# Optimization experiments

Hardware: AMD Instinct MI355X
Metric: run time of the kernel (lower is better)

Reference implementation:

```python
import jax, jax.numpy as jnp
import numpy as np

D = 1024      # d_model
H = 16        # nhead
DH = D // H   # head_dim = 64
ROT = DH // 2 # rotary_ndims = 32
FFN = 4096    # d_ffn
B, T, M, N = 4, 1024, 128, 64


def _layernorm(x, g, b, eps=1e-5):
    mu = jnp.mean(x, axis=-1, keepdims=True)
    var = jnp.mean(jnp.square(x - mu), axis=-1, keepdims=True)
    return (x - mu) * jax.lax.rsqrt(var + eps) * g + b


def _rotate_half(x):
    x1, x2 = x[..., : x.shape[-1] // 2], x[..., x.shape[-1] // 2:]
    return jnp.concatenate([-x2, x1], axis=-1)


def setup_inputs() -> dict:
    key = jax.random.key(0)
    ks = jax.random.split(key, 16)
    s = 0.02
    inp = {
        'x': jax.random.normal(ks[0], (B, T, D), jnp.float32),
        'memory': jax.random.normal(ks[1], (B, M, D), jnp.float32),
        'nmr': jax.random.normal(ks[2], (B, N, D), jnp.float32),
        'Wq': jax.random.normal(ks[3], (D, D), jnp.float32) * s,
        'bq': jnp.zeros((D,), jnp.float32),
        'Wk': jax.random.normal(ks[4], (D, D), jnp.float32) * s,
        'bk': jnp.zeros((D,), jnp.float32),
        'Wv': jax.random.normal(ks[5], (D, D), jnp.float32) * s,
        'bv': jnp.zeros((D,), jnp.float32),
        'Wo': jax.random.normal(ks[6], (D, D), jnp.float32) * s,
        'bo': jnp.zeros((D,), jnp.float32),
        'W1': jax.random.normal(ks[7], (D, FFN), jnp.float32) * s,
        'b1': jnp.zeros((FFN,), jnp.float32),
        'W2': jax.random.normal(ks[8], (FFN, D), jnp.float32) * s,
        'b2': jnp.zeros((D,), jnp.float32),
        'ln1_g': jnp.ones((D,), jnp.float32),
        'ln1_b': jnp.zeros((D,), jnp.float32),
        'ln2_g': jnp.ones((D,), jnp.float32),
        'ln2_b': jnp.zeros((D,), jnp.float32),
    }
    return inp


def reference(x, memory, nmr, Wq, bq, Wk, bk, Wv, bv, Wo, bo, W1, b1, W2, b2,
              ln1_g, ln1_b, ln2_g, ln2_b):
    b, t, _ = x.shape
    m, n = memory.shape[1], nmr.shape[1]
    pref = m + n
    L = pref + t

    x_full = jnp.concatenate([memory, nmr, x], axis=1)  # (B, L, D)
    xa = _layernorm(x_full, ln1_g, ln1_b)

    def heads(w, bias):
        return (xa @ w + bias).reshape(b, L, H, DH).transpose(0, 2, 1, 3)  # (B,H,L,DH)

    q = heads(Wq, bq)
    k = heads(Wk, bk)
    v = heads(Wv, bv)

    # partial RoPE on first ROT dims of each head
    pos = jnp.arange(L, dtype=jnp.float32)
    inv_freq = 1.0 / (10000.0 ** (jnp.arange(0, ROT, 2, dtype=jnp.float32) / ROT))
    freqs = pos[:, None] * inv_freq[None, :]              # (L, ROT/2)
    emb = jnp.concatenate([freqs, freqs], axis=-1)        # (L, ROT)
    cos, sin = jnp.cos(emb), jnp.sin(emb)
    qr, qp = q[..., :ROT], q[..., ROT:]
    kr, kp = k[..., :ROT], k[..., ROT:]
    qr = qr * cos + _rotate_half(qr) * sin
    kr = kr * cos + _rotate_half(kr) * sin
    q = jnp.concatenate([qr, qp], axis=-1)
    k = jnp.concatenate([kr, kp], axis=-1)

    # block mask: prefix (memory+nmr) fully bidirectional, target causal,
    # target attends to full prefix, prefix does NOT attend to target.
    i = jnp.arange(L)
    allowed = (i[None, :] < pref) | ((i[:, None] >= pref) & (i[None, :] >= pref)
                                     & (i[None, :] <= i[:, None]))  # (L, L)

    scale = 1.0 / jnp.sqrt(jnp.asarray(DH, jnp.float32))
    scores = jnp.einsum('bhqd,bhkd->bhqk', q, k) * scale
    scores = jnp.where(allowed[None, None], scores, jnp.finfo(scores.dtype).min)
    probs = jax.nn.softmax(scores, axis=-1)
    attn = jnp.einsum('bhqk,bhkd->bhqd', probs, v)        # (B,H,L,DH)
    attn = attn.transpose(0, 2, 1, 3).reshape(b, L, D)

    x_full = attn @ Wo + bo + x_full

    xf = _layernorm(x_full, ln2_g, ln2_b)
    xf = jnp.square(jax.nn.relu(xf @ W1 + b1)) @ W2 + b2
    x_full = x_full + xf

    return x_full[:, pref:]
```

## Files before the change

kernel.cpp:

```cpp
#include <hip/hip_runtime.h>
#include <hip/hip_bf16.h>
#include <math.h>

#define D_   1024
#define H_   16
#define DH_  64
#define FFN_ 4096
#define B_   4
#define T_   1024
#define M_   128
#define N_   64
#define PREF 192
#define L_   1216
#define BL_  (B_*L_)
#define BT_  (B_*T_)

typedef __attribute__((ext_vector_type(4))) float f32x4;
typedef __attribute__((ext_vector_type(8))) short bf16x8;
typedef __attribute__((ext_vector_type(8))) unsigned short u16x8;
typedef const __attribute__((address_space(1))) void gvoid_t;
typedef __attribute__((address_space(3))) void lvoid_t;

#define LGKM0 asm volatile("s_waitcnt lgkmcnt(0)" ::: "memory")

__device__ __forceinline__ void gl_lds16(const void* g, void* l) {
    __builtin_amdgcn_global_load_lds((gvoid_t*)g, (lvoid_t*)l, 16, 0, 0);
}

__device__ __forceinline__ ushort f2bf(float x) {
    union { __hip_bfloat16 h; ushort u; } cv;
    cv.h = __float2bfloat16(x);
    return cv.u;
}

__device__ __forceinline__ u16x8 pack8(float4 a, float4 b) {
    u16x8 r;
    r[0]=f2bf(a.x); r[1]=f2bf(a.y); r[2]=f2bf(a.z); r[3]=f2bf(a.w);
    r[4]=f2bf(b.x); r[5]=f2bf(b.y); r[6]=f2bf(b.z); r[7]=f2bf(b.w);
    return r;
}

__device__ __forceinline__ float block_reduce_sum256(float v, float* sbuf) {
#pragma unroll
    for (int o = 32; o > 0; o >>= 1) v += __shfl_xor(v, o, 64);
    int w = threadIdx.x >> 6;
    if ((threadIdx.x & 63) == 0) sbuf[w] = v;
    __syncthreads();
    float r = sbuf[0] + sbuf[1] + sbuf[2] + sbuf[3];
    __syncthreads();
    return r;
}

__device__ __forceinline__ void wtr_body(const float* __restrict__ W,
                                         ushort* __restrict__ Wt, int K, int Nc)
{
    __shared__ float tl[64][65];
    int c0 = blockIdx.x << 6, k0 = blockIdx.y << 6;
    int tid = threadIdx.x;
    int rr = tid >> 4, c4 = (tid & 15) << 2;
#pragma unroll
    for (int p = 0; p < 4; ++p) {
        int r = (p << 4) + rr;
        float4 v = *(const float4*)(W + (size_t)(k0 + r) * Nc + c0 + c4);
        tl[r][c4+0] = v.x; tl[r][c4+1] = v.y; tl[r][c4+2] = v.z; tl[r][c4+3] = v.w;
    }
    __syncthreads();
#pragma unroll
    for (int p = 0; p < 4; ++p) {
        int rT = (p << 4) + rr;
        ushort4 uv;
        uv.x = f2bf(tl[c4+0][rT]);
        uv.y = f2bf(tl[c4+1][rT]);
        uv.z = f2bf(tl[c4+2][rT]);
        uv.w = f2bf(tl[c4+3][rT]);
        *(ushort4*)(Wt + (size_t)(c0 + rT) * K + k0 + c4) = uv;
    }
}

__global__ __launch_bounds__(256) void wtr_kernel(
    const float* __restrict__ W, ushort* __restrict__ Wt, int K, int Nc)
{ wtr_body(W, Wt, K, Nc); }

__global__ __launch_bounds__(256) void wtr4_kernel(
    const float* __restrict__ W0, const float* __restrict__ W1,
    const float* __restrict__ W2, const float* __restrict__ W3,
    ushort* __restrict__ T0, ushort* __restrict__ T1,
    ushort* __restrict__ T2, ushort* __restrict__ T3)
{
    const float* W; ushort* T;
    switch (blockIdx.z) {
        case 0: W = W0; T = T0; break;
        case 1: W = W1; T = T1; break;
        case 2: W = W2; T = T2; break;
        default: W = W3; T = T3; break;
    }
    wtr_body(W, T, D_, D_);
}

__global__ __launch_bounds__(256) void prep_kernel(
    float* __restrict__ tab, const float* __restrict__ bq,
    const float* __restrict__ bk, const float* __restrict__ bv,
    float* __restrict__ ob)
{
    int i = blockIdx.x * 256 + threadIdx.x;
    if (i < L_ * 32) {
        int pos = i >> 5, idx = i & 31;
        int fi = idx & 15;
        float invf = exp2f(-(float)fi * 0.83048202372f);
        float th = (float)pos * invf;
        tab[i] = (idx < 16) ? cosf(th) : sinf(th);
    } else {
        int j = i - L_ * 32;
        if (j < 3072) {
            float v = (j < 1024) ? bq[j] : (j < 2048 ? bk[j - 1024] : bv[j - 2048]);
            ob[j] = v;
        }
    }
}

__global__ __launch_bounds__(256) void ln1_concat_kernel(
    const float* __restrict__ x, const float* __restrict__ mem,
    const float* __restrict__ nmr, const float* __restrict__ g,
    const float* __restrict__ be, float* __restrict__ x_full,
    ushort* __restrict__ xa_bf)
{
    __shared__ float sbuf[4];
    int row = blockIdx.x;
    int b = row / L_, pos = row % L_;
    const float* src;
    if (pos < M_)          src = mem + ((size_t)b*M_ + pos)      * D_;
    else if (pos < M_+N_)  src = nmr + ((size_t)b*N_ + (pos-M_)) * D_;
    else                   src = x   + ((size_t)b*T_ + (pos-PREF))*D_;

    int c = threadIdx.x << 2;
    float4 v = *(const float4*)(src + c);
    float s = v.x + v.y + v.z + v.w;
    s = block_reduce_sum256(s, sbuf);
    float mu = s * (1.0f / D_);
    float dx = v.x - mu, dy = v.y - mu, dz = v.z - mu, dw = v.w - mu;
    float q = dx*dx + dy*dy + dz*dz + dw*dw;
    q = block_reduce_sum256(q, sbuf);
    float inv = rsqrtf(q * (1.0f / D_) + 1e-5f);
    float4 gv = *(const float4*)(g + c);
    float4 bv = *(const float4*)(be + c);
    ushort4 o;
    o.x = f2bf(dx*inv*gv.x + bv.x);
    o.y = f2bf(dy*inv*gv.y + bv.y);
    o.z = f2bf(dz*inv*gv.z + bv.z);
    o.w = f2bf(dw*inv*gv.w + bv.w);
    *(float4*)(x_full + (size_t)row*D_ + c) = v;
    *(ushort4*)(xa_bf + (size_t)row*D_ + c) = o;
}

__global__ __launch_bounds__(256) void ln2_kernel(
    const float* __restrict__ src, const float* __restrict__ g,
    const float* __restrict__ be, ushort* __restrict__ dst)
{
    __shared__ float sbuf[4];
    int row = blockIdx.x;
    int c = threadIdx.x << 2;
    float4 v = *(const float4*)(src + (size_t)row*D_ + c);
    float s = v.x + v.y + v.z + v.w;
    s = block_reduce_sum256(s, sbuf);
    float mu = s * (1.0f / D_);
    float dx = v.x - mu, dy = v.y - mu, dz = v.z - mu, dw = v.w - mu;
    float q = dx*dx + dy*dy + dz*dz + dw*dw;
    q = block_reduce_sum256(q, sbuf);
    float inv = rsqrtf(q * (1.0f / D_) + 1e-5f);
    float4 gv = *(const float4*)(g + c);
    float4 bv = *(const float4*)(be + c);
    ushort4 o;
    o.x = f2bf(dx*inv*gv.x + bv.x);
    o.y = f2bf(dy*inv*gv.y + bv.y);
    o.z = f2bf(dz*inv*gv.z + bv.z);
    o.w = f2bf(dw*inv*gv.w + bv.w);
    *(ushort4*)(dst + (size_t)row*D_ + c) = o;
}

__global__ __launch_bounds__(256) void gemm_bf16_kernel(
    const ushort* __restrict__ A, const ushort* __restrict__ Bt,
    const float* __restrict__ bias, const float* __restrict__ rtab,
    void* __restrict__ Cout, int Nc, int Kstride, int Klen, int mode)
{
    __shared__ ushort SM[16384];
    int tid = threadIdx.x;
    int lane = tid & 63, w = tid >> 6;
    int wm = w >> 1, wn = w & 1;
    int nx = gridDim.x;
    int flat = blockIdx.y * nx + blockIdx.x;
    int cpx = (nx * gridDim.y) >> 3;
    int sz = (flat & 7) * cpx + (flat >> 3);
    int row0 = (sz / nx) << 7, col0 = (sz % nx) << 7;
    int l15 = lane & 15, l4 = lane >> 4;

    f32x4 acc[4][4] = {};

    int r_a = tid >> 2;
    int sc  = tid & 3;
    int lcOff = (sc ^ ((r_a >> 1) & 3)) << 3;
    const ushort* Arow  = A  + (size_t)(row0 + r_a)      * Kstride;
    const ushort* Arow2 = A  + (size_t)(row0 + 64 + r_a) * Kstride;
    const ushort* Brow  = Bt + (size_t)(col0 + r_a)      * Kstride;
    const ushort* Brow2 = Bt + (size_t)(col0 + 64 + r_a) * Kstride;

#define STAGE(buf, k0rel)                                                          \
    do {                                                                           \
        gl_lds16(Arow  + (k0rel) + lcOff, (char*)(SM + (buf)*4096) + (tid << 4));  \
        gl_lds16(Arow2 + (k0rel) + lcOff, (char*)(SM + (buf)*4096) + ((256+tid) << 4)); \
        gl_lds16(Brow  + (k0rel) + lcOff, (char*)(SM + 8192 + (buf)*4096) + (tid << 4)); \
        gl_lds16(Brow2 + (k0rel) + lcOff, (char*)(SM + 8192 + (buf)*4096) + ((256+tid) << 4)); \
    } while (0)

    STAGE(0, 0);
    __syncthreads();
    int cur = 0;
    for (int k0 = 0; k0 < Klen; k0 += 32) {
        if (k0 + 32 < Klen) STAGE(cur ^ 1, k0 + 32);
        const ushort* As = SM + cur*4096;
        const ushort* Bs = SM + 8192 + cur*4096;
        bf16x8 af[4], bfr[4];
#pragma unroll
        for (int i = 0; i < 4; ++i) {
            int ra = (wm << 6) + (i << 4) + l15;
            af[i]  = *(const bf16x8*)(&As[ra*32 + ((l4 ^ ((ra >> 1) & 3)) << 3)]);
            int rb = (wn << 6) + (i << 4) + l15;
            bfr[i] = *(const bf16x8*)(&Bs[rb*32 + ((l4 ^ ((rb >> 1) & 3)) << 3)]);
        }
#pragma unroll
        for (int i = 0; i < 4; ++i)
#pragma unroll
            for (int j = 0; j < 4; ++j)
                acc[i][j] = __builtin_amdgcn_mfma_f32_16x16x32_bf16(af[i], bfr[j], acc[i][j], 0, 0, 0);
        __syncthreads();
        cur ^= 1;
    }
#undef STAGE

    float bcol[4];
#pragma unroll
    for (int j = 0; j < 4; ++j) bcol[j] = bias[col0 + (wn << 6) + (j << 4) + l15];

    float* scr = (float*)SM + w * 1088;
    int rr = lane >> 2, cseg = lane & 3;
    int hh = ((col0 & 1023) + (wn << 6)) >> 6;
    int which = col0 >> 10;

#pragma unroll
    for (int i = 0; i < 4; ++i) {
        LGKM0;
#pragma unroll
        for (int j = 0; j < 4; ++j)
#pragma unroll
            for (int r = 0; r < 4; ++r)
                scr[((l4 << 2) + r)*68 + (j << 4) + l15] = acc[i][j][r] + bcol[j];
        LGKM0;
        int grow = row0 + (wm << 6) + (i << 4) + rr;

        if (which == 2) {
            int r0g = row0 + (wm << 6) + (i << 4);
            int bb = r0g / L_;
            int posb = r0g - bb * L_;
            float4 v0, v1, v2, v3;
            v0.x = scr[ 0*68 + lane]; v0.y = scr[ 1*68 + lane];
            v0.z = scr[ 2*68 + lane]; v0.w = scr[ 3*68 + lane];
            v1.x = scr[ 4*68 + lane]; v1.y = scr[ 5*68 + lane];
            v1.z = scr[ 6*68 + lane]; v1.w = scr[ 7*68 + lane];
            v2.x = scr[ 8*68 + lane]; v2.y = scr[ 9*68 + lane];
            v2.z = scr[10*68 + lane]; v2.w = scr[11*68 + lane];
            v3.x = scr[12*68 + lane]; v3.y = scr[13*68 + lane];
            v3.z = scr[14*68 + lane]; v3.w = scr[15*68 + lane];
            ushort* O = (ushort*)Cout + 2*(size_t)BL_*D_;
            size_t base = ((size_t)(bb*H_ + hh)*64 + lane)*L_ + posb;
            *(u16x8*)(O + base)     = pack8(v0, v1);
            *(u16x8*)(O + base + 8) = pack8(v2, v3);
        } else {
            int bb = grow / L_;
            int pos = grow - bb * L_;
            float4 a0 = *(float4*)&scr[rr*68 + (cseg << 4) + 0];
            float4 a1 = *(float4*)&scr[rr*68 + (cseg << 4) + 4];
            float4 a2 = *(float4*)&scr[rr*68 + (cseg << 4) + 8];
            float4 a3 = *(float4*)&scr[rr*68 + (cseg << 4) + 12];
            if (cseg < 2) {
                int oseg = cseg ^ 1;
                float4 p0 = *(float4*)&scr[rr*68 + (oseg << 4) + 0];
                float4 p1 = *(float4*)&scr[rr*68 + (oseg << 4) + 4];
                float4 p2 = *(float4*)&scr[rr*68 + (oseg << 4) + 8];
                float4 p3 = *(float4*)&scr[rr*68 + (oseg << 4) + 12];
                const float* tb = rtab + pos*32;
                float4 c0 = *(const float4*)(tb + 0),  c1 = *(const float4*)(tb + 4);
                float4 c2 = *(const float4*)(tb + 8),  c3 = *(const float4*)(tb + 12);
                float4 s0 = *(const float4*)(tb + 16), s1 = *(const float4*)(tb + 20);
                float4 s2 = *(const float4*)(tb + 24), s3 = *(const float4*)(tb + 28);
                float sg = (cseg == 0) ? -1.f : 1.f;
                a0.x = a0.x*c0.x + sg*p0.x*s0.x; a0.y = a0.y*c0.y + sg*p0.y*s0.y;
                a0.z = a0.z*c0.z + sg*p0.z*s0.z; a0.w = a0.w*c0.w + sg*p0.w*s0.w;
                a1.x = a1.x*c1.x + sg*p1.x*s1.x; a1.y = a1.y*c1.y + sg*p1.y*s1.y;
                a1.z = a1.z*c1.z + sg*p1.z*s1.z; a1.w = a1.w*c1.w + sg*p1.w*s1.w;
                a2.x = a2.x*c2.x + sg*p2.x*s2.x; a2.y = a2.y*c2.y + sg*p2.y*s2.y;
                a2.z = a2.z*c2.z + sg*p2.z*s2.z; a2.w = a2.w*c2.w + sg*p2.w*s2.w;
                a3.x = a3.x*c3.x + sg*p3.x*s3.x; a3.y = a3.y*c3.y + sg*p3.y*s3.y;
                a3.z = a3.z*c3.z + sg*p3.z*s3.z; a3.w = a3.w*c3.w + sg*p3.w*s3.w;
            }
            ushort* O = (ushort*)Cout + (size_t)which * ((size_t)BL_*D_);
            size_t base = (((size_t)(bb*H_ + hh)*L_ + pos) << 6) + (cseg << 4);
            *(u16x8*)(O + base)     = pack8(a0, a1);
            *(u16x8*)(O + base + 8) = pack8(a2, a3);
        }
    }
}

template<int KG>
__global__ __launch_bounds__(512) void gemm512_kernel(
    const ushort* __restrict__ A, const ushort* __restrict__ Bt,
    const float* __restrict__ bias, const float* __restrict__ res,
    void* __restrict__ Cout, int Nc, int Kstride, int Klen, int mode)
{
    constexpr int TN  = (KG == 1) ? 256 : 128;
    constexpr int SMU = (KG == 1) ? 24576 : 34816;
    __shared__ ushort SM[SMU];
    char* SMb = (char*)SM;

    int tid = threadIdx.x;
    int lane = tid & 63, w = tid >> 6;
    int l15 = lane & 15, l4 = lane >> 4;

    int nx = gridDim.x;
    int flat = blockIdx.y * nx + blockIdx.x;
    int cpx = (nx * gridDim.y) >> 3;
    int sz = (flat & 7) * cpx + (flat >> 3);
    int row0 = (sz / nx) << 7, col0 = (sz % nx) * TN;

    int wm, wn, g;
    if (KG == 1) { g = 0; wm = w >> 2; wn = w & 3; }
    else         { g = w >> 2; wm = (w >> 1) & 1; wn = w & 1; }

    f32x4 acc[4][4] = {};
    const int kl = (KG == 2) ? (Klen >> 1) : Klen;
    const int kb = (KG == 2) ? g * kl : 0;

    int cur = 0;
    if (KG == 1) {
        int rA = tid >> 2, scA = tid & 3;
        int lcA = (scA ^ ((rA >> 1) & 3)) << 3;
        const ushort* Ar = A + (size_t)(row0 + rA) * Kstride + lcA;
        int lcB1 = (scA ^ (((128 + rA) >> 1) & 3)) << 3;
        const ushort* Br0 = Bt + (size_t)(col0 + rA)       * Kstride + lcA;
        const ushort* Br1 = Bt + (size_t)(col0 + 128 + rA) * Kstride + lcB1;
#define STG1(buf, k0rel)                                                        \
        do {                                                                    \
            gl_lds16(Ar  + (k0rel), SMb + (buf)*8192 + (tid << 4));             \
            gl_lds16(Br0 + (k0rel), SMb + 16384 + (buf)*16384 + (tid << 4));    \
            gl_lds16(Br1 + (k0rel), SMb + 16384 + (buf)*16384 + 8192 + (tid << 4)); \
        } while (0)
        STG1(0, 0);
        __syncthreads();
        for (int k0 = 0; k0 < kl; k0 += 32) {
            if (k0 + 32 < kl) STG1(cur ^ 1, k0 + 32);
            const ushort* As = (const ushort*)(SMb + cur*8192);
            const ushort* Bs = (const ushort*)(SMb + 16384 + cur*16384);
            bf16x8 af[4], bfr[4];
#pragma unroll
            for (int i = 0; i < 4; ++i) {
                int ra = (wm << 6) + (i << 4) + l15;
                af[i]  = *(const bf16x8*)(&As[ra*32 + ((l4 ^ ((ra >> 1) & 3)) << 3)]);
                int rb = (wn << 6) + (i << 4) + l15;
                bfr[i] = *(const bf16x8*)(&Bs[rb*32 + ((l4 ^ ((rb >> 1) & 3)) << 3)]);
            }
#pragma unroll
            for (int i = 0; i < 4; ++i)
#pragma unroll
                for (int j = 0; j < 4; ++j)
                    acc[i][j] = __builtin_amdgcn_mfma_f32_16x16x32_bf16(af[i], bfr[j], acc[i][j], 0, 0, 0);
            __syncthreads();
            cur ^= 1;
        }
#undef STG1
    } else {
        int gt = tid & 255;
        int rA = gt >> 2, scA = gt & 3;
        int lc = (scA ^ ((rA >> 1) & 3)) << 3;
        const ushort* Ar0 = A  + (size_t)(row0 + rA)      * Kstride + kb + lc;
        const ushort* Ar1 = A  + (size_t)(row0 + 64 + rA) * Kstride + kb + lc;
        const ushort* Br0 = Bt + (size_t)(col0 + rA)      * Kstride + kb + lc;
        const ushort* Br1 = Bt + (size_t)(col0 + 64 + rA) * Kstride + kb + lc;
#define STG2(buf, k0rel)                                                        \
        do { int rbase = (g*2 + (buf)) * 8192;                                  \
            gl_lds16(Ar0 + (k0rel), SMb + rbase + (gt << 4));                   \
            gl_lds16(Ar1 + (k0rel), SMb + rbase + 4096 + (gt << 4));            \
            gl_lds16(Br0 + (k0rel), SMb + 32768 + rbase + (gt << 4));           \
            gl_lds16(Br1 + (k0rel), SMb + 32768 + rbase + 4096 + (gt << 4));    \
        } while (0)
        STG2(0, 0);
        __syncthreads();
        for (int k0 = 0; k0 < kl; k0 += 32) {
            if (k0 + 32 < kl) STG2(cur ^ 1, k0 + 32);
            const ushort* As = (const ushort*)(SMb + (g*2 + cur)*8192);
            const ushort* Bs = (const ushort*)(SMb + 32768 + (g*2 + cur)*8192);
            bf16x8 af[4], bfr[4];
#pragma unroll
            for (int i = 0; i < 4; ++i) {
                int ra = (wm << 6) + (i << 4) + l15;
                af[i]  = *(const bf16x8*)(&As[ra*32 + ((l4 ^ ((ra >> 1) & 3)) << 3)]);
                int rb = (wn << 6) + (i << 4) + l15;
                bfr[i] = *(const bf16x8*)(&Bs[rb*32 + ((l4 ^ ((rb >> 1) & 3)) << 3)]);
            }
#pragma unroll
            for (int i = 0; i < 4; ++i)
#pragma unroll
                for (int j = 0; j < 4; ++j)
                    acc[i][j] = __builtin_amdgcn_mfma_f32_16x16x32_bf16(af[i], bfr[j], acc[i][j], 0, 0, 0);
            __syncthreads();
            cur ^= 1;
        }
#undef STG2
    }

    float* scr;
    if (KG == 1) scr = (float*)SMb + w * 1088;
    else         scr = (float*)SMb + (w & 3) * (64 * 68);

    if (KG == 2) {
        if (g == 1) {
#pragma unroll
            for (int i = 0; i < 4; ++i)
#pragma unroll
                for (int j = 0; j < 4; ++j)
#pragma unroll
                    for (int r = 0; r < 4; ++r)
                        scr[((i << 4) + (l4 << 2) + r)*68 + (j << 4) + l15] = acc[i][j][r];
        }
        __syncthreads();
        if (g == 1) return;
#pragma unroll
        for (int i = 0; i < 4; ++i)
#pragma unroll
            for (int j = 0; j < 4; ++j)
#pragma unroll
                for (int r = 0; r < 4; ++r)
                    acc[i][j][r] += scr[((i << 4) + (l4 << 2) + r)*68 + (j << 4) + l15];
    }

    float bcol[4];
#pragma unroll
    for (int j = 0; j < 4; ++j) bcol[j] = bias[col0 + (wn << 6) + (j << 4) + l15];
    int rr = lane >> 2, cseg = lane & 3;
    int colbase = col0 + (wn << 6);

#pragma unroll
    for (int i = 0; i < 4; ++i) {
        LGKM0;
#pragma unroll
        for (int j = 0; j < 4; ++j)
#pragma unroll
            for (int r = 0; r < 4; ++r) {
                float v = acc[i][j][r] + bcol[j];
                if (mode == 3) { v = fmaxf(v, 0.f); v *= v; }
                scr[((l4 << 2) + r)*68 + (j << 4) + l15] = v;
            }
        LGKM0;
        int grow = row0 + (wm << 6) + (i << 4) + rr;
        float4 q0 = *(float4*)&scr[rr*68 + (cseg << 4) + 0];
        float4 q1 = *(float4*)&scr[rr*68 + (cseg << 4) + 4];
        float4 q2 = *(float4*)&scr[rr*68 + (cseg << 4) + 8];
        float4 q3 = *(float4*)&scr[rr*68 + (cseg << 4) + 12];
        int gcol = colbase + (cseg << 4);
        if (mode == 3) {
            ushort* O = (ushort*)Cout;
            *(u16x8*)(O + (size_t)grow*Nc + gcol)     = pack8(q0, q1);
            *(u16x8*)(O + (size_t)grow*Nc + gcol + 8) = pack8(q2, q3);
        } else {
            size_t roff;
            if (mode == 2) {
                int rs = (grow >> 10)*L_ + PREF + (grow & (T_-1));
                roff = (size_t)rs*D_ + gcol;
            } else {
                roff = (size_t)grow*Nc + gcol;
            }
            float4 r0 = *(const float4*)(res + roff);
            float4 r1 = *(const float4*)(res + roff + 4);
            float4 r2 = *(const float4*)(res + roff + 8);
            float4 r3 = *(const float4*)(res + roff + 12);
            q0.x += r0.x; q0.y += r0.y; q0.z += r0.z; q0.w += r0.w;
            q1.x += r1.x; q1.y += r1.y; q1.z += r1.z; q1.w += r1.w;
            q2.x += r2.x; q2.y += r2.y; q2.z += r2.z; q2.w += r2.w;
            q3.x += r3.x; q3.y += r3.y; q3.z += r3.z; q3.w += r3.w;
            float* O = (float*)Cout;
            size_t o = (size_t)grow*Nc + gcol;
            *(float4*)(O + o)      = q0;
            *(float4*)(O + o + 4)  = q1;
            *(float4*)(O + o + 8)  = q2;
            *(float4*)(O + o + 12) = q3;
        }
    }
}

__global__ __launch_bounds__(256) void attn_mfma_kernel(
    const ushort* __restrict__ qhd, const ushort* __restrict__ khd,
    const ushort* __restrict__ vt, ushort* __restrict__ attn_bf)
{
    __shared__ ushort Ks[2][64*64];
    __shared__ ushort Vs[2][64*64];
    __shared__ ushort Ps[4*16*64];

    int bid0 = blockIdx.x;
    int bid = (bid0 & 7) * (gridDim.x >> 3) + (bid0 >> 3);
    int qb = 15 - (bid & 15);
    int h  = (bid >> 4) & (H_ - 1);
    int b  = bid >> 8;
    int tid = threadIdx.x, lane = tid & 63, w = tid >> 6;
    int l15 = lane & 15, lg = lane >> 4;
    int i0 = PREF + (qb << 6);
    int wq0 = w << 4;
    size_t bh = (size_t)(b * H_ + h);

    const ushort* qrow = qhd + (bh * L_ + i0 + wq0 + l15) * 64;
    bf16x8 bq0 = *(const bf16x8*)(qrow + (lg << 3));
    bf16x8 bq1 = *(const bf16x8*)(qrow + 32 + (lg << 3));

    f32x4 acc[4] = {};
    float mrun = -INFINITY;
    float lsum = 0.f;

    int srow = tid >> 3;
    int sslot = tid & 7;
    ushort* Ps_w = Ps + (w << 10);
    const float SC = 0.125f * 1.4426950408889634f;
    int qcap = i0 + wq0 + l15;

#define STAGE_T(buf, t)                                                     \
    do { int j0s = (t) << 6;                                                \
        gl_lds16(khd + (bh * L_ + j0s + srow) * 64 + ((sslot ^ (srow & 7)) << 3),      \
                 (char*)Ks[buf] + (tid << 4));                              \
        gl_lds16(khd + (bh * L_ + j0s + 32 + srow) * 64 + ((sslot ^ ((32+srow) & 7)) << 3), \
                 (char*)Ks[buf] + ((256 + tid) << 4));                      \
        gl_lds16(vt + (bh * 64 + srow) * L_ + j0s + ((sslot ^ (srow & 7)) << 3),       \
                 (char*)Vs[buf] + (tid << 4));                              \
        gl_lds16(vt + (bh * 64 + 32 + srow) * L_ + j0s + ((sslot ^ ((32+srow) & 7)) << 3), \
                 (char*)Vs[buf] + ((256 + tid) << 4));                      \
    } while (0)

    int ntile = 4 + qb;
    STAGE_T(0, 0);
    __syncthreads();
    int cur = 0;
    for (int t = 0; t < ntile; ++t) {
        if (t + 1 < ntile) STAGE_T(cur ^ 1, t + 1);
        const ushort* Kc = Ks[cur];
        const ushort* Vc = Vs[cur];

        f32x4 s4[4];
        __builtin_amdgcn_s_setprio(1);
#pragma unroll
        for (int st = 0; st < 4; ++st) {
            int rk = (st << 4) + l15;
            bf16x8 ak0 = *(const bf16x8*)(Kc + (rk << 6) + ((lg       ^ (rk & 7)) << 3));
            bf16x8 ak1 = *(const bf16x8*)(Kc + (rk << 6) + (((4 + lg) ^ (rk & 7)) << 3));
            f32x4 z = {};
            z = __builtin_amdgcn_mfma_f32_16x16x32_bf16(ak0, bq0, z, 0, 0, 0);
            z = __builtin_amdgcn_mfma_f32_16x16x32_bf16(ak1, bq1, z, 0, 0, 0);
            s4[st] = z;
        }
        __builtin_amdgcn_s_setprio(0);

        int j0 = t << 6;
        float sv[4][4];
        bool diag = (t == ntile - 1);
        int kbq = j0 + (lg << 2);
#pragma unroll
        for (int st = 0; st < 4; ++st)
#pragma unroll
            for (int r = 0; r < 4; ++r) {
                float s = s4[st][r] * SC;
                if (diag && (kbq + (st << 4) + r > qcap)) s = -INFINITY;
                sv[st][r] = s;
            }
        float bm;
        {
            float t0 = fmaxf(fmaxf(sv[0][0], sv[0][1]), fmaxf(sv[0][2], sv[0][3]));
            float t1 = fmaxf(fmaxf(sv[1][0], sv[1][1]), fmaxf(sv[1][2], sv[1][3]));
            float t2 = fmaxf(fmaxf(sv[2][0], sv[2][1]), fmaxf(sv[2][2], sv[2][3]));
            float t3 = fmaxf(fmaxf(sv[3][0], sv[3][1]), fmaxf(sv[3][2], sv[3][3]));
            bm = fmaxf(fmaxf(t0, t1), fmaxf(t2, t3));
        }
        bm = fmaxf(bm, __shfl_xor(bm, 16, 64));
        bm = fmaxf(bm, __shfl_xor(bm, 32, 64));

        float mn = fmaxf(mrun, bm);
        float cr = exp2f(mrun - mn);
        mrun = mn;
        float pe[4][4];
        float ps = 0.f;
#pragma unroll
        for (int st = 0; st < 4; ++st)
#pragma unroll
            for (int r = 0; r < 4; ++r) {
                float e = exp2f(sv[st][r] - mn);
                pe[st][r] = e; ps += e;
            }
        ps += __shfl_xor(ps, 16, 64);
        ps += __shfl_xor(ps, 32, 64);
        lsum = lsum * cr + ps;
#pragma unroll
        for (int su = 0; su < 4; ++su) acc[su] *= cr;

#pragma unroll
        for (int st = 0; st < 4; ++st) {
            int slot = (st << 1) + (lg >> 1);
            int sb = ((lg & 1) << 3);
#pragma unroll
            for (int rp = 0; rp < 2; ++rp) {
                uint u = (uint)f2bf(pe[st][2*rp]) | ((uint)f2bf(pe[st][2*rp+1]) << 16);
                *(uint*)((char*)Ps_w + l15*128 + ((slot ^ (l15 & 7)) << 4) + sb + (rp << 2)) = u;
            }
        }
        {
            bf16x8 bp0 = *(const bf16x8*)((char*)Ps_w + l15*128 + ((lg       ^ (l15 & 7)) << 4));
            bf16x8 bp1 = *(const bf16x8*)((char*)Ps_w + l15*128 + (((4 + lg) ^ (l15 & 7)) << 4));
            __builtin_amdgcn_s_setprio(1);
#pragma unroll
            for (int su = 0; su < 4; ++su) {
                int rd = (su << 4) + l15;
                bf16x8 av0 = *(const bf16x8*)(Vc + (rd << 6) + ((lg       ^ (rd & 7)) << 3));
                bf16x8 av1 = *(const bf16x8*)(Vc + (rd << 6) + (((4 + lg) ^ (rd & 7)) << 3));
                acc[su] = __builtin_amdgcn_mfma_f32_16x16x32_bf16(av0, bp0, acc[su], 0, 0, 0);
                acc[su] = __builtin_amdgcn_mfma_f32_16x16x32_bf16(av1, bp1, acc[su], 0, 0, 0);
            }
            __builtin_amdgcn_s_setprio(0);
        }
        __syncthreads();
        cur ^= 1;
    }
#undef STAGE_T

    float rl = 1.0f / lsum;
    size_t orow = (size_t)b * T_ + (i0 - PREF) + wq0 + l15;
#pragma unroll
    for (int su = 0; su < 4; ++su) {
        ushort4 o4;
        o4.x = f2bf(acc[su][0] * rl);
        o4.y = f2bf(acc[su][1] * rl);
        o4.z = f2bf(acc[su][2] * rl);
        o4.w = f2bf(acc[su][3] * rl);
        *(ushort4*)(attn_bf + orow * D_ + (h << 6) + (su << 4) + (lg << 2)) = o4;
    }
}

extern "C" void kernel_launch(void* const* d_in, const int* in_sizes, int n_in,
                              void* d_out, int out_size, void* d_ws, size_t ws_size,
                              hipStream_t stream) {
    const float* x   = (const float*)d_in[0];
    const float* mem = (const float*)d_in[1];
    const float* nmr = (const float*)d_in[2];
    const float* Wq  = (const float*)d_in[3];
    const float* bq  = (const float*)d_in[4];
    const float* Wk  = (const float*)d_in[5];
    const float* bk  = (const float*)d_in[6];
    const float* Wv  = (const float*)d_in[7];
    const float* bv  = (const float*)d_in[8];
    const float* Wo  = (const float*)d_in[9];
    const float* bo  = (const float*)d_in[10];
    const float* W1  = (const float*)d_in[11];
    const float* b1  = (const float*)d_in[12];
    const float* W2  = (const float*)d_in[13];
    const float* b2  = (const float*)d_in[14];
    const float* g1  = (const float*)d_in[15];
    const float* be1 = (const float*)d_in[16];
    const float* g2  = (const float*)d_in[17];
    const float* be2 = (const float*)d_in[18];
    float* out = (float*)d_out;

    const size_t BLD = (size_t)BL_ * D_;
    const size_t BTD = (size_t)BT_ * D_;

    float* f = (float*)d_ws;
    float* x_full = f;
    float* x2     = f + BLD;
    float* bqkv   = x2 + BTD;
    float* rtab   = bqkv + 4096;
    ushort* bfb   = (ushort*)(rtab + (size_t)L_*32);
    ushort* xa_bf   = bfb;
    ushort* qhd     = bfb + BLD;
    ushort* khd     = bfb + 2*BLD;
    ushort* vt      = bfb + 3*BLD;
    ushort* h1_bf   = bfb + 4*BLD;
    ushort* wq_bf = h1_bf + (size_t)BT_*FFN_;
    ushort* wk_bf = wq_bf + (size_t)D_*D_;
    ushort* wv_bf = wk_bf + (size_t)D_*D_;
    ushort* wo_bf = wv_bf + (size_t)D_*D_;
    ushort* w1_bf = wo_bf + (size_t)D_*D_;
    ushort* w2_bf = w1_bf + (size_t)D_*FFN_;
    ushort* attn_bf = xa_bf;
    ushort* ln2_bf  = qhd;

    wtr4_kernel<<<dim3(16, 16, 4), 256, 0, stream>>>(Wq, Wk, Wv, Wo,
                                                     wq_bf, wk_bf, wv_bf, wo_bf);
    wtr_kernel<<<dim3(FFN_/64, D_/64),   256, 0, stream>>>(W1, w1_bf, D_,   FFN_);
    wtr_kernel<<<dim3(D_/64,   FFN_/64), 256, 0, stream>>>(W2, w2_bf, FFN_, D_);
    prep_kernel<<<(L_*32 + 3072 + 255)/256, 256, 0, stream>>>(rtab, bq, bk, bv, bqkv);

    ln1_concat_kernel<<<BL_, 256, 0, stream>>>(x, mem, nmr, g1, be1, x_full, xa_bf);

    gemm_bf16_kernel<<<dim3(3072/128, BL_/128), 256, 0, stream>>>(
        xa_bf, wq_bf, bqkv, rtab, qhd, D_, D_, D_, 7);

    attn_mfma_kernel<<<B_*H_*(T_/64), 256, 0, stream>>>(qhd, khd, vt, attn_bf);

    gemm512_kernel<2><<<dim3(D_/128, BT_/128), 512, 0, stream>>>(
        attn_bf, wo_bf, bo, x_full, x2, D_, D_, D_, 2);

    ln2_kernel<<<BT_, 256, 0, stream>>>(x2, g2, be2, ln2_bf);

    gemm512_kernel<1><<<dim3(FFN_/256, BT_/128), 512, 0, stream>>>(
        ln2_bf, w1_bf, b1, nullptr, h1_bf, FFN_, D_, D_, 3);

    gemm512_kernel<2><<<dim3(D_/128, BT_/128), 512, 0, stream>>>(
        h1_bf, w2_bf, b2, x2, out, D_, FFN_, FFN_, 1);
}
```

Measured before the change: 254.2 us.

## Split split-K GEMM into 256-thread 128x64 tile kernel with doubled grid

Replaces the templated 512-thread GEMM with two specialised kernels. The FFN1 path keeps its 128x256 tile with the mode branches removed. The Wo and FFN2 split-K GEMMs move to a new 256-thread kernel with a 128x64 output tile, two K-halves of two warps each, and reduction through LDS. This doubles the block count for the N=1024 GEMMs to improve CU occupancy and load balance, at the cost of less B-tile reuse per block and more A traffic.

```diff
diff --git a/kernel.cpp b/kernel.cpp
--- a/kernel.cpp
+++ b/kernel.cpp
@@ -309,15 +309,12 @@
     }
 }
 
-template<int KG>
-__global__ __launch_bounds__(512) void gemm512_kernel(
+__global__ __launch_bounds__(512) void gemm_ffn1_kernel(
     const ushort* __restrict__ A, const ushort* __restrict__ Bt,
-    const float* __restrict__ bias, const float* __restrict__ res,
-    void* __restrict__ Cout, int Nc, int Kstride, int Klen, int mode)
-{
-    constexpr int TN  = (KG == 1) ? 256 : 128;
-    constexpr int SMU = (KG == 1) ? 24576 : 34816;
-    __shared__ ushort SM[SMU];
+    const float* __restrict__ bias, void* __restrict__ Cout,
+    int Nc, int Kstride, int Klen)
+{
+    __shared__ ushort SM[24576];
     char* SMb = (char*)SM;
 
     int tid = threadIdx.x;
@@ -328,121 +325,54 @@
     int flat = blockIdx.y * nx + blockIdx.x;
     int cpx = (nx * gridDim.y) >> 3;
     int sz = (flat & 7) * cpx + (flat >> 3);
-    int row0 = (sz / nx) << 7, col0 = (sz % nx) * TN;
-
-    int wm, wn, g;
-    if (KG == 1) { g = 0; wm = w >> 2; wn = w & 3; }
-    else         { g = w >> 2; wm = (w >> 1) & 1; wn = w & 1; }
+    int row0 = (sz / nx) << 7, col0 = (sz % nx) << 8;
+
+    int wm = w >> 2, wn = w & 3;
 
     f32x4 acc[4][4] = {};
-    const int kl = (KG == 2) ? (Klen >> 1) : Klen;
-    const int kb = (KG == 2) ? g * kl : 0;
-
+
+    int rA = tid >> 2, scA = tid & 3;
+    int lcA = (scA ^ ((rA >> 1) & 3)) << 3;
+    const ushort* Ar = A + (size_t)(row0 + rA) * Kstride + lcA;
+    int lcB1 = (scA ^ (((128 + rA) >> 1) & 3)) << 3;
+    const ushort* Br0 = Bt + (size_t)(col0 + rA)       * Kstride + lcA;
+    const ushort* Br1 = Bt + (size_t)(col0 + 128 + rA) * Kstride + lcB1;
+#define STG1(buf, k0rel)                                                        \
+    do {                                                                        \
+        gl_lds16(Ar  + (k0rel), SMb + (buf)*8192 + (tid << 4));                 \
+        gl_lds16(Br0 + (k0rel), SMb + 16384 + (buf)*16384 + (tid << 4));        \
+        gl_lds16(Br1 + (k0rel), SMb + 16384 + (buf)*16384 + 8192 + (tid << 4)); \
+    } while (0)
+    STG1(0, 0);
+    __syncthreads();
     int cur = 0;
-    if (KG == 1) {
-        int rA = tid >> 2, scA = tid & 3;
-        int lcA = (scA ^ ((rA >> 1) & 3)) << 3;
-        const ushort* Ar = A + (size_t)(row0 + rA) * Kstride + lcA;
-        int lcB1 = (scA ^ (((128 + rA) >> 1) & 3)) << 3;
-        const ushort* Br0 = Bt + (size_t)(col0 + rA)       * Kstride + lcA;
-        const ushort* Br1 = Bt + (size_t)(col0 + 128 + rA) * Kstride + lcB1;
-#define STG1(buf, k0rel)                                                        \
-        do {                                                                    \
-            gl_lds16(Ar  + (k0rel), SMb + (buf)*8192 + (tid << 4));             \
-            gl_lds16(Br0 + (k0rel), SMb + 16384 + (buf)*16384 + (tid << 4));    \
-            gl_lds16(Br1 + (k0rel), SMb + 16384 + (buf)*16384 + 8192 + (tid << 4)); \
-        } while (0)
-        STG1(0, 0);
+    for (int k0 = 0; k0 < Klen; k0 += 32) {
+        if (k0 + 32 < Klen) STG1(cur ^ 1, k0 + 32);
+        const ushort* As = (const ushort*)(SMb + cur*8192);
+        const ushort* Bs = (const ushort*)(SMb + 16384 + cur*16384);
+        bf16x8 af[4], bfr[4];
+#pragma unroll
+        for (int i = 0; i < 4; ++i) {
+            int ra = (wm << 6) + (i << 4) + l15;
+            af[i]  = *(const bf16x8*)(&As[ra*32 + ((l4 ^ ((ra >> 1) & 3)) << 3)]);
+            int rb = (wn << 6) + (i << 4) + l15;
+            bfr[i] = *(const bf16x8*)(&Bs[rb*32 + ((l4 ^ ((rb >> 1) & 3)) << 3)]);
+        }
+#pragma unroll
+        for (int i = 0; i < 4; ++i)
+#pragma unroll
+            for (int j = 0; j < 4; ++j)
+                acc[i][j] = __builtin_amdgcn_mfma_f32_16x16x32_bf16(af[i], bfr[j], acc[i][j], 0, 0, 0);
         __syncthreads();
-        for (int k0 = 0; k0 < kl; k0 += 32) {
-            if (k0 + 32 < kl) STG1(cur ^ 1, k0 + 32);
-            const ushort* As = (const ushort*)(SMb + cur*8192);
-            const ushort* Bs = (const ushort*)(SMb + 16384 + cur*16384);
-            bf16x8 af[4], bfr[4];
-#pragma unroll
-            for (int i = 0; i < 4; ++i) {
-                int ra = (wm << 6) + (i << 4) + l15;
-                af[i]  = *(const bf16x8*)(&As[ra*32 + ((l4 ^ ((ra >> 1) & 3)) << 3)]);
-                int rb = (wn << 6) + (i << 4) + l15;
-                bfr[i] = *(const bf16x8*)(&Bs[rb*32 + ((l4 ^ ((rb >> 1) & 3)) << 3)]);
-            }
-#pragma unroll
-            for (int i = 0; i < 4; ++i)
-#pragma unroll
-                for (int j = 0; j < 4; ++j)
-                    acc[i][j] = __builtin_amdgcn_mfma_f32_16x16x32_bf16(af[i], bfr[j], acc[i][j], 0, 0, 0);
-            __syncthreads();
-            cur ^= 1;
-        }
+        cur ^= 1;
+    }
 #undef STG1
-    } else {
-        int gt = tid & 255;
-        int rA = gt >> 2, scA = gt & 3;
-        int lc = (scA ^ ((rA >> 1) & 3)) << 3;
-        const ushort* Ar0 = A  + (size_t)(row0 + rA)      * Kstride + kb + lc;
-        const ushort* Ar1 = A  + (size_t)(row0 + 64 + rA) * Kstride + kb + lc;
-        const ushort* Br0 = Bt + (size_t)(col0 + rA)      * Kstride + kb + lc;
-        const ushort* Br1 = Bt + (size_t)(col0 + 64 + rA) * Kstride + kb + lc;
-#define STG2(buf, k0rel)                                                        \
-        do { int rbase = (g*2 + (buf)) * 8192;                                  \
-            gl_lds16(Ar0 + (k0rel), SMb + rbase + (gt << 4));                   \
-            gl_lds16(Ar1 + (k0rel), SMb + rbase + 4096 + (gt << 4));            \
-            gl_lds16(Br0 + (k0rel), SMb + 32768 + rbase + (gt << 4));           \
-            gl_lds16(Br1 + (k0rel), SMb + 32768 + rbase + 4096 + (gt << 4));    \
-        } while (0)
-        STG2(0, 0);
-        __syncthreads();
-        for (int k0 = 0; k0 < kl; k0 += 32) {
-            if (k0 + 32 < kl) STG2(cur ^ 1, k0 + 32);
-            const ushort* As = (const ushort*)(SMb + (g*2 + cur)*8192);
-            const ushort* Bs = (const ushort*)(SMb + 32768 + (g*2 + cur)*8192);
-            bf16x8 af[4], bfr[4];
-#pragma unroll
-            for (int i = 0; i < 4; ++i) {
-                int ra = (wm << 6) + (i << 4) + l15;
-                af[i]  = *(const bf16x8*)(&As[ra*32 + ((l4 ^ ((ra >> 1) & 3)) << 3)]);
-                int rb = (wn << 6) + (i << 4) + l15;
-                bfr[i] = *(const bf16x8*)(&Bs[rb*32 + ((l4 ^ ((rb >> 1) & 3)) << 3)]);
-            }
-#pragma unroll
-            for (int i = 0; i < 4; ++i)
-#pragma unroll
-                for (int j = 0; j < 4; ++j)
-                    acc[i][j] = __builtin_amdgcn_mfma_f32_16x16x32_bf16(af[i], bfr[j], acc[i][j], 0, 0, 0);
-            __syncthreads();
-            cur ^= 1;
-        }
-#undef STG2
-    }
-
-    float* scr;
-    if (KG == 1) scr = (float*)SMb + w * 1088;
-    else         scr = (float*)SMb + (w & 3) * (64 * 68);
-
-    if (KG == 2) {
-        if (g == 1) {
-#pragma unroll
-            for (int i = 0; i < 4; ++i)
-#pragma unroll
-                for (int j = 0; j < 4; ++j)
-#pragma unroll
-                    for (int r = 0; r < 4; ++r)
-                        scr[((i << 4) + (l4 << 2) + r)*68 + (j << 4) + l15] = acc[i][j][r];
-        }
-        __syncthreads();
-        if (g == 1) return;
-#pragma unroll
-        for (int i = 0; i < 4; ++i)
-#pragma unroll
-            for (int j = 0; j < 4; ++j)
-#pragma unroll
-                for (int r = 0; r < 4; ++r)
-                    acc[i][j][r] += scr[((i << 4) + (l4 << 2) + r)*68 + (j << 4) + l15];
-    }
 
     float bcol[4];
 #pragma unroll
     for (int j = 0; j < 4; ++j) bcol[j] = bias[col0 + (wn << 6) + (j << 4) + l15];
+
+    float* scr = (float*)SMb + w * 1088;
     int rr = lane >> 2, cseg = lane & 3;
     int colbase = col0 + (wn << 6);
 
@@ -454,7 +384,7 @@
 #pragma unroll
             for (int r = 0; r < 4; ++r) {
                 float v = acc[i][j][r] + bcol[j];
-                if (mode == 3) { v = fmaxf(v, 0.f); v *= v; }
+                v = fmaxf(v, 0.f); v *= v;
                 scr[((l4 << 2) + r)*68 + (j << 4) + l15] = v;
             }
         LGKM0;
@@ -464,33 +394,143 @@
         float4 q2 = *(float4*)&scr[rr*68 + (cseg << 4) + 8];
         float4 q3 = *(float4*)&scr[rr*68 + (cseg << 4) + 12];
         int gcol = colbase + (cseg << 4);
-        if (mode == 3) {
-            ushort* O = (ushort*)Cout;
-            *(u16x8*)(O + (size_t)grow*Nc + gcol)     = pack8(q0, q1);
-            *(u16x8*)(O + (size_t)grow*Nc + gcol + 8) = pack8(q2, q3);
+        ushort* O = (ushort*)Cout;
+        *(u16x8*)(O + (size_t)grow*Nc + gcol)     = pack8(q0, q1);
+        *(u16x8*)(O + (size_t)grow*Nc + gcol + 8) = pack8(q2, q3);
+    }
+}
+
+__global__ __launch_bounds__(256) void gemm_sk2_kernel(
+    const ushort* __restrict__ A, const ushort* __restrict__ Bt,
+    const float* __restrict__ bias, const float* __restrict__ res,
+    float* __restrict__ Cout, int Nc, int Kstride, int Klen, int mode)
+{
+    __shared__ ushort SM[24576];
+    char* SMb = (char*)SM;
+    int tid = threadIdx.x;
+    int lane = tid & 63, w = tid >> 6;
+    int l15 = lane & 15, l4 = lane >> 4;
+    int g = w >> 1, wm = w & 1;
+
+    int nx = gridDim.x;
+    int flat = blockIdx.y * nx + blockIdx.x;
+    int cpx = (nx * gridDim.y) >> 3;
+    int sz = (flat & 7) * cpx + (flat >> 3);
+    int row0 = (sz / nx) << 7, col0 = (sz % nx) << 6;
+
+    f32x4 acc[4][4] = {};
+    const int kl = Klen >> 1;
+    const int kb = g * kl;
+
+    int gt = tid & 127;
+    int rB = gt >> 2, sc = gt & 3;
+    const ushort* Abase = A  + (size_t)row0 * Kstride + kb;
+    const ushort* Bbase = Bt + (size_t)col0 * Kstride + kb;
+    char* AL = SMb + g * 16384;
+    char* BL = SMb + 32768 + g * 8192;
+
+#define STG2(buf, k0rel)                                                        \
+    do {                                                                        \
+        _Pragma("unroll")                                                       \
+        for (int p = 0; p < 4; ++p) {                                           \
+            int rw = (p << 5) + rB; int lc = sc ^ ((rw >> 1) & 3);              \
+            gl_lds16(Abase + (size_t)rw*Kstride + (k0rel) + (lc << 3),          \
+                     AL + (buf)*8192 + (p << 11) + (gt << 4));                  \
+        }                                                                       \
+        _Pragma("unroll")                                                       \
+        for (int p = 0; p < 2; ++p) {                                           \
+            int rw = (p << 5) + rB; int lc = sc ^ ((rw >> 1) & 3);              \
+            gl_lds16(Bbase + (size_t)rw*Kstride + (k0rel) + (lc << 3),          \
+                     BL + (buf)*4096 + (p << 11) + (gt << 4));                  \
+        }                                                                       \
+    } while (0)
+
+    STG2(0, 0);
+    __syncthreads();
+    int cur = 0;
+    for (int k0 = 0; k0 < kl; k0 += 32) {
+        if (k0 + 32 < kl) STG2(cur ^ 1, k0 + 32);
+        const ushort* As = (const ushort*)(AL + cur*8192);
+        const ushort* Bs = (const ushort*)(BL + cur*4096);
+        bf16x8 af[4], bfr[4];
+#pragma unroll
+        for (int i = 0; i < 4; ++i) {
+            int ra = (wm << 6) + (i << 4) + l15;
+            af[i]  = *(const bf16x8*)(&As[ra*32 + ((l4 ^ ((ra >> 1) & 3)) << 3)]);
+            int rb = (i << 4) + l15;
+            bfr[i] = *(const bf16x8*)(&Bs[rb*32 + ((l4 ^ ((rb >> 1) & 3)) << 3)]);
+        }
+#pragma unroll
+        for (int i = 0; i < 4; ++i)
+#pragma unroll
+            for (int j = 0; j < 4; ++j)
+                acc[i][j] = __builtin_amdgcn_mfma_f32_16x16x32_bf16(af[i], bfr[j], acc[i][j], 0, 0, 0);
+        __syncthreads();
+        cur ^= 1;
+    }
+#undef STG2
+
+    float* scr2 = (float*)SMb;
+    if (g == 1) {
+#pragma unroll
+        for (int i = 0; i < 4; ++i)
+#pragma unroll
+            for (int j = 0; j < 4; ++j)
+#pragma unroll
+                for (int r = 0; r < 4; ++r)
+                    scr2[((wm << 6) + (i << 4) + (l4 << 2) + r)*68 + (j << 4) + l15] = acc[i][j][r];
+    }
+    __syncthreads();
+    if (g == 1) return;
+#pragma unroll
+    for (int i = 0; i < 4; ++i)
+#pragma unroll
+        for (int j = 0; j < 4; ++j)
+#pragma unroll
+            for (int r = 0; r < 4; ++r)
+                acc[i][j][r] += scr2[((wm << 6) + (i << 4) + (l4 << 2) + r)*68 + (j << 4) + l15];
+
+    float bcol[4];
+#pragma unroll
+    for (int j = 0; j < 4; ++j) bcol[j] = bias[col0 + (j << 4) + l15];
+    int rr = lane >> 2, cseg = lane & 3;
+    float* scr = (float*)(SMb + 36864) + w * 1088;
+
+#pragma unroll
+    for (int i = 0; i < 4; ++i) {
+        LGKM0;
+#pragma unroll
+        for (int j = 0; j < 4; ++j)
+#pragma unroll
+            for (int r = 0; r < 4; ++r)
+                scr[((l4 << 2) + r)*68 + (j << 4) + l15] = acc[i][j][r] + bcol[j];
+        LGKM0;
+        int grow = row0 + (wm << 6) + (i << 4) + rr;
+        float4 q0 = *(float4*)&scr[rr*68 + (cseg << 4) + 0];
+        float4 q1 = *(float4*)&scr[rr*68 + (cseg << 4) + 4];
+        float4 q2 = *(float4*)&scr[rr*68 + (cseg << 4) + 8];
+        float4 q3 = *(float4*)&scr[rr*68 + (cseg << 4) + 12];
+        int gcol = col0 + (cseg << 4);
+        size_t roff;
+        if (mode == 2) {
+            int rs = (grow >> 10)*L_ + PREF + (grow & (T_-1));
+            roff = (size_t)rs*D_ + gcol;
         } else {
-            size_t roff;
-            if (mode == 2) {
-                int rs = (grow >> 10)*L_ + PREF + (grow & (T_-1));
-                roff = (size_t)rs*D_ + gcol;
-            } else {
-                roff = (size_t)grow*Nc + gcol;
-            }
-            float4 r0 = *(const float4*)(res + roff);
-            float4 r1 = *(const float4*)(res + roff + 4);
-            float4 r2 = *(const float4*)(res + roff + 8);
-            float4 r3 = *(const float4*)(res + roff + 12);
-            q0.x += r0.x; q0.y += r0.y; q0.z += r0.z; q0.w += r0.w;
-            q1.x += r1.x; q1.y += r1.y; q1.z += r1.z; q1.w += r1.w;
-            q2.x += r2.x; q2.y += r2.y; q2.z += r2.z; q2.w += r2.w;
-            q3.x += r3.x; q3.y += r3.y; q3.z += r3.z; q3.w += r3.w;
-            float* O = (float*)Cout;
-            size_t o = (size_t)grow*Nc + gcol;
-            *(float4*)(O + o)      = q0;
-            *(float4*)(O + o + 4)  = q1;
-            *(float4*)(O + o + 8)  = q2;
-            *(float4*)(O + o + 12) = q3;
-        }
+            roff = (size_t)grow*Nc + gcol;
+        }
+        float4 r0 = *(const float4*)(res + roff);
+        float4 r1 = *(const float4*)(res + roff + 4);
+        float4 r2 = *(const float4*)(res + roff + 8);
+        float4 r3 = *(const float4*)(res + roff + 12);
+        q0.x += r0.x; q0.y += r0.y; q0.z += r0.z; q0.w += r0.w;
+        q1.x += r1.x; q1.y += r1.y; q1.z += r1.z; q1.w += r1.w;
+        q2.x += r2.x; q2.y += r2.y; q2.z += r2.z; q2.w += r2.w;
+        q3.x += r3.x; q3.y += r3.y; q3.z += r3.z; q3.w += r3.w;
+        size_t o = (size_t)grow*Nc + gcol;
+        *(float4*)(Cout + o)      = q0;
+        *(float4*)(Cout + o + 4)  = q1;
+        *(float4*)(Cout + o + 8)  = q2;
+        *(float4*)(Cout + o + 12) = q3;
     }
 }
 
@@ -705,14 +745,14 @@
 
     attn_mfma_kernel<<<B_*H_*(T_/64), 256, 0, stream>>>(qhd, khd, vt, attn_bf);
 
-    gemm512_kernel<2><<<dim3(D_/128, BT_/128), 512, 0, stream>>>(
+    gemm_sk2_kernel<<<dim3(D_/64, BT_/128), 256, 0, stream>>>(
         attn_bf, wo_bf, bo, x_full, x2, D_, D_, D_, 2);
 
     ln2_kernel<<<BT_, 256, 0, stream>>>(x2, g2, be2, ln2_bf);
 
-    gemm512_kernel<1><<<dim3(FFN_/256, BT_/128), 512, 0, stream>>>(
-        ln2_bf, w1_bf, b1, nullptr, h1_bf, FFN_, D_, D_, 3);
-
-    gemm512_kernel<2><<<dim3(D_/128, BT_/128), 512, 0, stream>>>(
+    gemm_ffn1_kernel<<<dim3(FFN_/256, BT_/128), 512, 0, stream>>>(
+        ln2_bf, w1_bf, b1, h1_bf, FFN_, D_, D_);
+
+    gemm_sk2_kernel<<<dim3(D_/64, BT_/128), 256, 0, stream>>>(
         h1_bf, w2_bf, b2, x2, out, D_, FFN_, FFN_, 1);
 }
```

After: 254.5 us. About the same (+0.1%).
